# Performance work log

Hardware: AMD Instinct MI355X
Metric: run time of the kernel (lower is better)

Reference implementation:

```python
import jax, jax.numpy as jnp
import numpy as np

EPS = 0.05
N = 33554432  # 2**25 annotation steps


def setup_inputs() -> dict:
    key = jax.random.key(0)
    # categories in 1..5 (cat==0 is a no-op skip in the original loop; excluding it
    # keeps the output length static at N+1)
    annotation_series = jax.random.randint(key, (N,), 1, 6, dtype=jnp.int64 if jax.config.jax_enable_x64 else jnp.int32)
    # learned scalar weights of the six Linear(1,1,bias=False) layers, at their init constants
    return {
        "annotation_series": annotation_series,
        "origin_w": jnp.asarray(0.0, jnp.float32),
        "big_decrease_w": jnp.asarray(-0.3, jnp.float32),
        "decrease_w": jnp.asarray(-0.1, jnp.float32),
        "same_w": jnp.asarray(0.0, jnp.float32),
        "increase_w": jnp.asarray(0.1, jnp.float32),
        "big_increase_w": jnp.asarray(0.3, jnp.float32),
    }


def _change_table(origin_w, bd, d, s, inc, bi):
    sg = jax.lax.stop_gradient  # clamp bounds came from .item() in torch -> detached
    c1 = jnp.minimum(bd, sg(jnp.minimum(0.0, d))) - EPS                 # big decrease
    c2 = jnp.clip(d, sg(bd) + EPS, 0.0 - EPS)                           # decrease
    c3 = s                                                              # same
    c4 = jnp.clip(inc, 0.0 + EPS, sg(bi) - EPS)                         # increase
    c5 = jnp.maximum(bi, sg(jnp.maximum(0.0, inc)) + EPS)               # big increase
    zero = jnp.zeros_like(c1)  # cat 0 unused (inputs restricted to 1..5)
    return jnp.stack([zero, c1, c2, c3, c4, c5])  # [6]


def reference(annotation_series, origin_w, big_decrease_w, decrease_w, same_w, increase_w, big_increase_w):
    table = _change_table(origin_w, big_decrease_w, decrease_w, same_w, increase_w, big_increase_w)
    changes = table[annotation_series]                    # [N] gather from 6-entry LUT
    series = origin_w + jnp.cumsum(changes)               # [N] inclusive prefix sum
    return jnp.concatenate([origin_w[None], series])      # [N+1]
```

## Files before the change

### kernel.cpp

```cpp
#include <hip/hip_runtime.h>

#define EPS_C 0.05f

typedef int i4 __attribute__((ext_vector_type(4)));
typedef float f4 __attribute__((ext_vector_type(4)));

__device__ __forceinline__ void build_table(const float* bd_p, const float* d_p,
                                            const float* s_p, const float* inc_p,
                                            const float* bi_p, float* cs) {
  if (threadIdx.x == 0) {
    float bd = *bd_p, d = *d_p, s = *s_p, inc = *inc_p, bi = *bi_p;
    cs[0] = 0.0f;
    cs[1] = fminf(bd, fminf(0.0f, d)) - EPS_C;
    cs[2] = fminf(fmaxf(d, bd + EPS_C), -EPS_C);
    cs[3] = s;
    cs[4] = fminf(fmaxf(inc, EPS_C), bi - EPS_C);
    cs[5] = fmaxf(bi, fmaxf(0.0f, inc) + EPS_C);
    cs[6] = 0.0f; cs[7] = 0.0f;
  }
}

__global__ __launch_bounds__(256) void k_pack_reduce(
    const int* __restrict__ ann, const float* bd, const float* d,
    const float* s, const float* inc, const float* bi,
    unsigned short* __restrict__ pack, float* __restrict__ fine) {
  __shared__ float cs[8];
  build_table(bd, d, s, inc, bi, cs);
  __syncthreads();
  const int t = threadIdx.x, lane = t & 63, w = t >> 6, b = blockIdx.x;
  const size_t ebase = (size_t)b * 8192 + w * 2048;
  const i4* in4 = (const i4*)ann + (ebase >> 2) + lane;
  unsigned short* pk = pack + (ebase >> 2) + lane;
  float fs0 = 0.0f, fs1 = 0.0f;
#pragma unroll
  for (int r = 0; r < 8; ++r) {
    i4 v = __builtin_nontemporal_load(&in4[r * 64]);
    float e = cs[v.x] + cs[v.y] + cs[v.z] + cs[v.w];
    if (r < 4) fs0 += e; else fs1 += e;
    unsigned us = (unsigned)v.x | ((unsigned)v.y << 4) |
                  ((unsigned)v.z << 8) | ((unsigned)v.w << 12);
    pk[r * 64] = (unsigned short)us;
  }
#pragma unroll
  for (int off = 32; off >= 1; off >>= 1) {
    fs0 += __shfl_xor(fs0, off, 64);
    fs1 += __shfl_xor(fs1, off, 64);
  }
  if (lane == 0) {
    fine[b * 8 + w * 2 + 0] = fs0;
    fine[b * 8 + w * 2 + 1] = fs1;
  }
}

__global__ __launch_bounds__(1024) void k_scan_fine(
    const float* __restrict__ fine, const float* __restrict__ origin,
    float* __restrict__ pref, float* __restrict__ outN) {
  __shared__ float ws[16];
  const int t = threadIdx.x, lane = t & 63, w = t >> 6;
  float v[32];
  const f4* fv = (const f4*)fine + t * 8;
  float tot = 0.0f;
#pragma unroll
  for (int i = 0; i < 8; ++i) {
    f4 x = fv[i];
    v[i * 4 + 0] = x.x; v[i * 4 + 1] = x.y;
    v[i * 4 + 2] = x.z; v[i * 4 + 3] = x.w;
    tot += x.x + x.y + x.z + x.w;
  }
  float x = tot;
#pragma unroll
  for (int off = 1; off < 64; off <<= 1) {
    float y = __shfl_up(x, off, 64);
    if (lane >= off) x += y;
  }
  if (lane == 63) ws[w] = x;
  __syncthreads();
  float wexcl = 0.0f;
#pragma unroll
  for (int i = 0; i < 16; ++i) { float wv = ws[i]; if (i < w) wexcl += wv; }
  float run = *origin + wexcl + (x - tot);
#pragma unroll
  for (int i = 0; i < 8; ++i) {
    f4 o;
    o.x = run; run += v[i * 4 + 0];
    o.y = run; run += v[i * 4 + 1];
    o.z = run; run += v[i * 4 + 2];
    o.w = run; run += v[i * 4 + 3];
    ((f4*)pref)[t * 8 + i] = o;
  }
  if (t == 1023) *outN = run;
}

__global__ __launch_bounds__(256) void k_scan_out(
    const unsigned short* __restrict__ pack, const float* __restrict__ pref,
    const float* bd, const float* d, const float* s, const float* inc,
    const float* bi, float* __restrict__ out) {
  __shared__ float cs[8];
  build_table(bd, d, s, inc, bi, cs);
  __syncthreads();
  const int t = threadIdx.x, lane = t & 63, w = t >> 6, b = blockIdx.x;
#pragma unroll
  for (int h = 0; h < 2; ++h) {
    const int u = b * 8 + w * 2 + h;
    const size_t ebase = (size_t)u * 1024;
    const unsigned short* pk = pack + (ebase >> 2) + lane;
    unsigned short us0 = pk[0], us1 = pk[64], us2 = pk[128], us3 = pk[192];
    float carry = pref[u];
    unsigned short usv[4] = {us0, us1, us2, us3};
#pragma unroll
    for (int r = 0; r < 4; ++r) {
      const unsigned us = usv[r];
      const float v0 = cs[us & 0xFu];
      const float v1 = cs[(us >> 4) & 0xFu];
      const float v2 = cs[(us >> 8) & 0xFu];
      const float v3 = cs[(us >> 12) & 0xFu];
      const float s4 = v0 + v1 + v2 + v3;
      float x = s4;
#pragma unroll
      for (int off = 1; off < 64; off <<= 1) {
        float y = __shfl_up(x, off, 64);
        if (lane >= off) x += y;
      }
      const float off0 = carry + (x - s4);
      f4 o;
      o.x = off0;
      o.y = off0 + v0;
      o.z = o.y + v1;
      o.w = o.z + v2;
      __builtin_nontemporal_store(o, (f4*)(out + ebase + r * 256 + lane * 4));
      carry += __shfl(x, 63, 64);
    }
  }
}

extern "C" void kernel_launch(void* const* d_in, const int* in_sizes, int n_in,
                              void* d_out, int out_size, void* d_ws, size_t ws_size,
                              hipStream_t stream) {
  const int*   ann    = (const int*)d_in[0];
  const float* origin = (const float*)d_in[1];
  const float* bd     = (const float*)d_in[2];
  const float* dw     = (const float*)d_in[3];
  const float* sw     = (const float*)d_in[4];
  const float* ic     = (const float*)d_in[5];
  const float* bi     = (const float*)d_in[6];
  float* out = (float*)d_out;

  const int N   = in_sizes[0];
  const int nb  = N / 8192;
  const int nf  = N / 1024;

  float* fine = (float*)d_ws;
  float* pref = fine + nf;
  unsigned short* pack = (unsigned short*)(pref + nf);

  k_pack_reduce<<<nb, 256, 0, stream>>>(ann, bd, dw, sw, ic, bi, pack, fine);
  k_scan_fine<<<1, 1024, 0, stream>>>(fine, origin, pref, out + N);
  k_scan_out<<<nb, 256, 0, stream>>>(pack, pref, bd, dw, sw, ic, bi, out);
}
```

Before: 248.1 us.

## Fuse pack, scan, and output into one cooperative kernel with grid sync

Replaces the three-kernel pipeline with a single cooperative kernel when N matches the expected size. Each block reads its annotations once, keeps the packed nibbles in registers, and publishes its block sum. After a grid-wide sync it computes its exclusive prefix from the other blocks' sums and writes the scanned output. This removes the packed intermediate buffer round trip and two extra launches, including the single-block scan. In exchange it adds grid sync overhead, higher register use, and reliance on all blocks being co-resident, with the old path kept as a fallback.

```diff
diff --git a/kernel.cpp b/kernel.cpp
--- a/kernel.cpp
+++ b/kernel.cpp
@@ -1,6 +1,12 @@
 #include <hip/hip_runtime.h>
+#include <hip/hip_cooperative_groups.h>
+
+namespace cg = cooperative_groups;
 
 #define EPS_C 0.05f
+#define BLOCK 256
+#define BPB   32768
+#define NB    1024
 
 typedef int i4 __attribute__((ext_vector_type(4)));
 typedef float f4 __attribute__((ext_vector_type(4)));
@@ -20,6 +26,106 @@
   }
 }
 
+__global__ __launch_bounds__(BLOCK, 4) void k_fused(
+    const int* __restrict__ ann, const float* __restrict__ origin,
+    const float* bd, const float* d, const float* s, const float* inc,
+    const float* bi, float* __restrict__ out, float* __restrict__ coarse,
+    int nb) {
+  __shared__ float cs[8];
+  __shared__ float wsum[4];
+  __shared__ float ws2[4];
+  __shared__ float s_excl;
+  const int t = threadIdx.x, lane = t & 63, w = t >> 6, b = blockIdx.x;
+
+  build_table(bd, d, s, inc, bi, cs);
+  __syncthreads();
+
+  const size_t ebase = (size_t)b * BPB + (size_t)w * 8192;
+  const i4* in4 = (const i4*)ann + (ebase >> 2) + lane;
+  unsigned pk[16];
+  float usum[8];
+#pragma unroll
+  for (int u = 0; u < 8; ++u) {
+    float sum = 0.0f;
+#pragma unroll
+    for (int r = 0; r < 4; ++r) {
+      i4 v = __builtin_nontemporal_load(&in4[u * 256 + r * 64]);
+      sum += cs[v.x] + cs[v.y] + cs[v.z] + cs[v.w];
+      unsigned nib = (unsigned)v.x | ((unsigned)v.y << 4) |
+                     ((unsigned)v.z << 8) | ((unsigned)v.w << 12);
+      if (r & 1) pk[u * 2 + (r >> 1)] |= nib << 16;
+      else       pk[u * 2 + (r >> 1)]  = nib;
+    }
+#pragma unroll
+    for (int off = 32; off >= 1; off >>= 1) sum += __shfl_xor(sum, off, 64);
+    usum[u] = sum;
+  }
+  float wtot = 0.0f;
+#pragma unroll
+  for (int u = 0; u < 8; ++u) wtot += usum[u];
+  if (lane == 0) wsum[w] = wtot;
+  __syncthreads();
+  if (t == 0) {
+    float bt = wsum[0] + wsum[1] + wsum[2] + wsum[3];
+    __hip_atomic_store(&coarse[b], bt, __ATOMIC_RELEASE,
+                       __HIP_MEMORY_SCOPE_AGENT);
+  }
+
+  cg::this_grid().sync();
+
+  float p = 0.0f;
+  for (int i = t; i < b; i += BLOCK)
+    p += __hip_atomic_load(&coarse[i], __ATOMIC_RELAXED,
+                           __HIP_MEMORY_SCOPE_AGENT);
+#pragma unroll
+  for (int off = 32; off >= 1; off >>= 1) p += __shfl_xor(p, off, 64);
+  if (lane == 0) ws2[w] = p;
+  __syncthreads();
+  if (t == 0) {
+    float e = *origin + ws2[0] + ws2[1] + ws2[2] + ws2[3];
+    s_excl = e;
+    if (b == nb - 1)
+      out[(size_t)nb * BPB] = e + wsum[0] + wsum[1] + wsum[2] + wsum[3];
+  }
+  __syncthreads();
+
+  float carry = s_excl;
+  if (w > 0) carry += wsum[0];
+  if (w > 1) carry += wsum[1];
+  if (w > 2) carry += wsum[2];
+#pragma unroll
+  for (int u = 0; u < 8; ++u) {
+    float c2 = carry;
+#pragma unroll
+    for (int r = 0; r < 4; ++r) {
+      const unsigned pw = pk[u * 2 + (r >> 1)];
+      const unsigned us = (r & 1) ? (pw >> 16) : (pw & 0xFFFFu);
+      const float v0 = cs[us & 0xFu];
+      const float v1 = cs[(us >> 4) & 0xFu];
+      const float v2 = cs[(us >> 8) & 0xFu];
+      const float v3 = cs[(us >> 12) & 0xFu];
+      const float s4 = v0 + v1 + v2 + v3;
+      float x = s4;
+#pragma unroll
+      for (int off = 1; off < 64; off <<= 1) {
+        float y = __shfl_up(x, off, 64);
+        if (lane >= off) x += y;
+      }
+      const float off0 = c2 + (x - s4);
+      f4 o;
+      o.x = off0;
+      o.y = off0 + v0;
+      o.z = o.y + v1;
+      o.w = o.z + v2;
+      __builtin_nontemporal_store(
+          o, (f4*)(out + ebase + u * 1024 + r * 256 + lane * 4));
+      c2 += __shfl(x, 63, 64);
+    }
+    carry += usum[u];
+  }
+}
+
+
 __global__ __launch_bounds__(256) void k_pack_reduce(
     const int* __restrict__ ann, const float* bd, const float* d,
     const float* s, const float* inc, const float* bi,
@@ -30,7 +136,7 @@
   const int t = threadIdx.x, lane = t & 63, w = t >> 6, b = blockIdx.x;
   const size_t ebase = (size_t)b * 8192 + w * 2048;
   const i4* in4 = (const i4*)ann + (ebase >> 2) + lane;
-  unsigned short* pk = pack + (ebase >> 2) + lane;
+  unsigned short* pkp = pack + (ebase >> 2) + lane;
   float fs0 = 0.0f, fs1 = 0.0f;
 #pragma unroll
   for (int r = 0; r < 8; ++r) {
@@ -39,7 +145,7 @@
     if (r < 4) fs0 += e; else fs1 += e;
     unsigned us = (unsigned)v.x | ((unsigned)v.y << 4) |
                   ((unsigned)v.z << 8) | ((unsigned)v.w << 12);
-    pk[r * 64] = (unsigned short)us;
+    pkp[r * 64] = (unsigned short)us;
   }
 #pragma unroll
   for (int off = 32; off >= 1; off >>= 1) {
@@ -103,10 +209,9 @@
   for (int h = 0; h < 2; ++h) {
     const int u = b * 8 + w * 2 + h;
     const size_t ebase = (size_t)u * 1024;
-    const unsigned short* pk = pack + (ebase >> 2) + lane;
-    unsigned short us0 = pk[0], us1 = pk[64], us2 = pk[128], us3 = pk[192];
+    const unsigned short* pkp = pack + (ebase >> 2) + lane;
+    unsigned short usv[4] = {pkp[0], pkp[64], pkp[128], pkp[192]};
     float carry = pref[u];
-    unsigned short usv[4] = {us0, us1, us2, us3};
 #pragma unroll
     for (int r = 0; r < 4; ++r) {
       const unsigned us = usv[r];
@@ -145,15 +250,32 @@
   const float* bi     = (const float*)d_in[6];
   float* out = (float*)d_out;
 
-  const int N   = in_sizes[0];
-  const int nb  = N / 8192;
+  const int N = in_sizes[0];
+
+  float* coarse = (float*)d_ws;
+
+  if (N == NB * BPB) {
+    int maxb = 0;
+    hipError_t qe = hipOccupancyMaxActiveBlocksPerMultiprocessor(
+        &maxb, (const void*)k_fused, BLOCK, 0);
+    if (qe == hipSuccess && maxb >= 4) {
+      int nb = NB;
+      void* args[] = {(void*)&ann, (void*)&origin, (void*)&bd, (void*)&dw,
+                      (void*)&sw, (void*)&ic, (void*)&bi, (void*)&out,
+                      (void*)&coarse, (void*)&nb};
+      hipError_t e = hipLaunchCooperativeKernel((const void*)k_fused, dim3(NB),
+                                                dim3(BLOCK), args, 0, stream);
+      if (e == hipSuccess) return;
+    }
+  }
+
+  const int nbc = N / 8192;
   const int nf  = N / 1024;
-
-  float* fine = (float*)d_ws;
+  float* fine = (float*)d_ws + 4096;
   float* pref = fine + nf;
   unsigned short* pack = (unsigned short*)(pref + nf);
 
-  k_pack_reduce<<<nb, 256, 0, stream>>>(ann, bd, dw, sw, ic, bi, pack, fine);
+  k_pack_reduce<<<nbc, 256, 0, stream>>>(ann, bd, dw, sw, ic, bi, pack, fine);
   k_scan_fine<<<1, 1024, 0, stream>>>(fine, origin, pref, out + N);
-  k_scan_out<<<nb, 256, 0, stream>>>(pack, pref, bd, dw, sw, ic, bi, out);
-}
+  k_scan_out<<<nbc, 256, 0, stream>>>(pack, pref, bd, dw, sw, ic, bi, out);
+}
```

Result: no change. 248.9 us (+0.3%).

## Drop single-block scan kernel; each output block sums preceding block totals itself

Applied to the files above, without the earlier changes.

Removes the single-block k_scan_fine launch. The pack kernel now also writes a per-block coarse sum, and each output block computes its own exclusive prefix by summing every preceding coarse entry in parallel, then scans its 8 fine partials within the block. The packed nibbles are also stored as 64-bit u2 words, so each wave does one coalesced load per unit. This saves a kernel launch and the serial gap between the two stages. In exchange, later blocks re-read up to 4096 coarse values (redundant O(nb^2) total reads, mostly served from cache), and the prefix is summed in a different order, which can change floating-point rounding.

```diff
diff --git a/kernel.cpp b/kernel.cpp
--- a/kernel.cpp
+++ b/kernel.cpp
@@ -1,9 +1,12 @@
 #include <hip/hip_runtime.h>
 
 #define EPS_C 0.05f
+#define BLOCK 256
+#define BPB   8192
 
 typedef int i4 __attribute__((ext_vector_type(4)));
 typedef float f4 __attribute__((ext_vector_type(4)));
+typedef unsigned int u2 __attribute__((ext_vector_type(2)));
 
 __device__ __forceinline__ void build_table(const float* bd_p, const float* d_p,
                                             const float* s_p, const float* inc_p,
@@ -20,96 +23,87 @@
   }
 }
 
-__global__ __launch_bounds__(256) void k_pack_reduce(
+__global__ __launch_bounds__(BLOCK) void k_pack_reduce(
     const int* __restrict__ ann, const float* bd, const float* d,
     const float* s, const float* inc, const float* bi,
-    unsigned short* __restrict__ pack, float* __restrict__ fine) {
+    u2* __restrict__ pack, float* __restrict__ coarse,
+    float* __restrict__ fine) {
   __shared__ float cs[8];
+  __shared__ float wsum[4];
   build_table(bd, d, s, inc, bi, cs);
   __syncthreads();
   const int t = threadIdx.x, lane = t & 63, w = t >> 6, b = blockIdx.x;
-  const size_t ebase = (size_t)b * 8192 + w * 2048;
+  const size_t ebase = (size_t)b * BPB + (size_t)w * 2048;
   const i4* in4 = (const i4*)ann + (ebase >> 2) + lane;
-  unsigned short* pk = pack + (ebase >> 2) + lane;
-  float fs0 = 0.0f, fs1 = 0.0f;
+  float fs[2];
 #pragma unroll
-  for (int r = 0; r < 8; ++r) {
-    i4 v = __builtin_nontemporal_load(&in4[r * 64]);
-    float e = cs[v.x] + cs[v.y] + cs[v.z] + cs[v.w];
-    if (r < 4) fs0 += e; else fs1 += e;
-    unsigned us = (unsigned)v.x | ((unsigned)v.y << 4) |
-                  ((unsigned)v.z << 8) | ((unsigned)v.w << 12);
-    pk[r * 64] = (unsigned short)us;
-  }
+  for (int u = 0; u < 2; ++u) {
+    unsigned lo = 0, hi = 0;
+    float sum = 0.0f;
 #pragma unroll
-  for (int off = 32; off >= 1; off >>= 1) {
-    fs0 += __shfl_xor(fs0, off, 64);
-    fs1 += __shfl_xor(fs1, off, 64);
+    for (int r = 0; r < 4; ++r) {
+      i4 v = __builtin_nontemporal_load(&in4[u * 256 + r * 64]);
+      sum += cs[v.x] + cs[v.y] + cs[v.z] + cs[v.w];
+      unsigned nib = (unsigned)v.x | ((unsigned)v.y << 4) |
+                     ((unsigned)v.z << 8) | ((unsigned)v.w << 12);
+      if (r & 1) { if (r < 2) lo |= nib << 16; else hi |= nib << 16; }
+      else       { if (r < 2) lo |= nib;       else hi |= nib; }
+    }
+    pack[((size_t)b * 8 + w * 2 + u) * 64 + lane] = (u2){lo, hi};
+#pragma unroll
+    for (int off = 32; off >= 1; off >>= 1) sum += __shfl_xor(sum, off, 64);
+    fs[u] = sum;
   }
   if (lane == 0) {
-    fine[b * 8 + w * 2 + 0] = fs0;
-    fine[b * 8 + w * 2 + 1] = fs1;
+    fine[b * 8 + w * 2 + 0] = fs[0];
+    fine[b * 8 + w * 2 + 1] = fs[1];
+    wsum[w] = fs[0] + fs[1];
   }
+  __syncthreads();
+  if (t == 0) coarse[b] = wsum[0] + wsum[1] + wsum[2] + wsum[3];
 }
 
-__global__ __launch_bounds__(1024) void k_scan_fine(
+__global__ __launch_bounds__(BLOCK) void k_scan_out(
+    const u2* __restrict__ pack, const float* __restrict__ coarse,
     const float* __restrict__ fine, const float* __restrict__ origin,
-    float* __restrict__ pref, float* __restrict__ outN) {
-  __shared__ float ws[16];
-  const int t = threadIdx.x, lane = t & 63, w = t >> 6;
-  float v[32];
-  const f4* fv = (const f4*)fine + t * 8;
-  float tot = 0.0f;
+    const float* bd, const float* d, const float* s, const float* inc,
+    const float* bi, float* __restrict__ out, int nb) {
+  __shared__ float cs[8];
+  __shared__ float ws2[4];
+  build_table(bd, d, s, inc, bi, cs);
+  const int t = threadIdx.x, lane = t & 63, w = t >> 6, b = blockIdx.x;
+
+  const u2 pk0 = pack[((size_t)b * 8 + w * 2 + 0) * 64 + lane];
+  const u2 pk1 = pack[((size_t)b * 8 + w * 2 + 1) * 64 + lane];
+
+  float p = 0.0f;
+  for (int i = t; i < b; i += BLOCK) p += coarse[i];
 #pragma unroll
-  for (int i = 0; i < 8; ++i) {
-    f4 x = fv[i];
-    v[i * 4 + 0] = x.x; v[i * 4 + 1] = x.y;
-    v[i * 4 + 2] = x.z; v[i * 4 + 3] = x.w;
-    tot += x.x + x.y + x.z + x.w;
+  for (int off = 32; off >= 1; off >>= 1) p += __shfl_xor(p, off, 64);
+  if (lane == 0) ws2[w] = p;
+  __syncthreads();
+  const float P = *origin + ws2[0] + ws2[1] + ws2[2] + ws2[3];
+
+  float f = (lane < 8) ? fine[b * 8 + lane] : 0.0f;
+#pragma unroll
+  for (int off = 1; off < 8; off <<= 1) {
+    float y = __shfl_up(f, off, 64);
+    if (lane >= off && lane < 8) f += y;
   }
-  float x = tot;
-#pragma unroll
-  for (int off = 1; off < 64; off <<= 1) {
-    float y = __shfl_up(x, off, 64);
-    if (lane >= off) x += y;
-  }
-  if (lane == 63) ws[w] = x;
-  __syncthreads();
-  float wexcl = 0.0f;
-#pragma unroll
-  for (int i = 0; i < 16; ++i) { float wv = ws[i]; if (i < w) wexcl += wv; }
-  float run = *origin + wexcl + (x - tot);
-#pragma unroll
-  for (int i = 0; i < 8; ++i) {
-    f4 o;
-    o.x = run; run += v[i * 4 + 0];
-    o.y = run; run += v[i * 4 + 1];
-    o.z = run; run += v[i * 4 + 2];
-    o.w = run; run += v[i * 4 + 3];
-    ((f4*)pref)[t * 8 + i] = o;
-  }
-  if (t == 1023) *outN = run;
-}
+  if (b == nb - 1 && w == 0 && lane == 7)
+    out[(size_t)nb * BPB] = P + f;
 
-__global__ __launch_bounds__(256) void k_scan_out(
-    const unsigned short* __restrict__ pack, const float* __restrict__ pref,
-    const float* bd, const float* d, const float* s, const float* inc,
-    const float* bi, float* __restrict__ out) {
-  __shared__ float cs[8];
-  build_table(bd, d, s, inc, bi, cs);
-  __syncthreads();
-  const int t = threadIdx.x, lane = t & 63, w = t >> 6, b = blockIdx.x;
+  const u2 pks[2] = {pk0, pk1};
 #pragma unroll
   for (int h = 0; h < 2; ++h) {
-    const int u = b * 8 + w * 2 + h;
-    const size_t ebase = (size_t)u * 1024;
-    const unsigned short* pk = pack + (ebase >> 2) + lane;
-    unsigned short us0 = pk[0], us1 = pk[64], us2 = pk[128], us3 = pk[192];
-    float carry = pref[u];
-    unsigned short usv[4] = {us0, us1, us2, us3};
+    const int j = w * 2 + h;
+    float carry = P + ((j > 0) ? __shfl(f, j - 1, 64) : 0.0f);
+    const u2 pk = pks[h];
+    const size_t ubase = (size_t)b * BPB + (size_t)j * 1024;
 #pragma unroll
     for (int r = 0; r < 4; ++r) {
-      const unsigned us = usv[r];
+      const unsigned pw = (r < 2) ? pk.x : pk.y;
+      const unsigned us = (r & 1) ? (pw >> 16) : (pw & 0xFFFFu);
       const float v0 = cs[us & 0xFu];
       const float v1 = cs[(us >> 4) & 0xFu];
       const float v2 = cs[(us >> 8) & 0xFu];
@@ -127,7 +121,7 @@
       o.y = off0 + v0;
       o.z = o.y + v1;
       o.w = o.z + v2;
-      __builtin_nontemporal_store(o, (f4*)(out + ebase + r * 256 + lane * 4));
+      __builtin_nontemporal_store(o, (f4*)(out + ubase + r * 256 + lane * 4));
       carry += __shfl(x, 63, 64);
     }
   }
@@ -145,15 +139,15 @@
   const float* bi     = (const float*)d_in[6];
   float* out = (float*)d_out;
 
-  const int N   = in_sizes[0];
-  const int nb  = N / 8192;
-  const int nf  = N / 1024;
+  const int N  = in_sizes[0];
+  const int nb = N / BPB;
 
-  float* fine = (float*)d_ws;
-  float* pref = fine + nf;
-  unsigned short* pack = (unsigned short*)(pref + nf);
+  float* coarse = (float*)d_ws;
+  float* fine   = coarse + 4096;
+  u2*    pack   = (u2*)(fine + 32768);
 
-  k_pack_reduce<<<nb, 256, 0, stream>>>(ann, bd, dw, sw, ic, bi, pack, fine);
-  k_scan_fine<<<1, 1024, 0, stream>>>(fine, origin, pref, out + N);
-  k_scan_out<<<nb, 256, 0, stream>>>(pack, pref, bd, dw, sw, ic, bi, out);
+  k_pack_reduce<<<nb, BLOCK, 0, stream>>>(ann, bd, dw, sw, ic, bi,
+                                          pack, coarse, fine);
+  k_scan_out<<<nb, BLOCK, 0, stream>>>(pack, coarse, fine, origin,
+                                       bd, dw, sw, ic, bi, out, nb);
 }
```

After: 241.1 us. -2.8%, faster.
